# Optimization experiments

Measured on AMD Instinct MI355X. Metric: run time of the kernel, lower is better.

## Reference

```python
import jax, jax.numpy as jnp
import numpy as np

DIM = 512
NUM_HEADS = 8
HEAD_DIM = DIM // NUM_HEADS
SCALE = HEAD_DIM ** -0.5
B, N = 8, 1024


def setup_inputs() -> dict:
    key = jax.random.key(0)
    k1, k2, k3, k4, k5 = jax.random.split(key, 5)
    x = jax.random.normal(k1, (B, N, DIM), dtype=jnp.float32)
    rpe_bias = jax.random.normal(k2, (1, NUM_HEADS, N, N), dtype=jnp.float32)
    # torch Linear weights: [out_features, in_features], y = x @ W.T
    qkv_w = jax.random.normal(k3, (3 * DIM, DIM), dtype=jnp.float32) * (DIM ** -0.5)
    proj_w = jax.random.normal(k4, (DIM, DIM), dtype=jnp.float32) * (DIM ** -0.5)
    proj_b = jax.random.normal(k5, (DIM,), dtype=jnp.float32) * 0.01
    return {"x": x, "rpe_bias": rpe_bias, "qkv_w": qkv_w, "proj_w": proj_w, "proj_b": proj_b}


def reference(x, rpe_bias, qkv_w, proj_w, proj_b):
    b, n, c = x.shape
    h, d = NUM_HEADS, HEAD_DIM
    # qkv projection (no bias): [B,N,3C] -> [3,B,H,N,D]
    qkv = (x @ qkv_w.T).reshape(b, n, 3, h, d).transpose(2, 0, 3, 1, 4)
    q, k, v = qkv[0], qkv[1], qkv[2]
    attn = jnp.einsum('bhnd,bhmd->bhnm', q, k) * SCALE + rpe_bias
    attn = jax.nn.softmax(attn, axis=-1)  # dropout p=0 -> identity
    out = jnp.einsum('bhnm,bhmd->bhnd', attn, v)
    out = out.transpose(0, 2, 1, 3).reshape(b, n, c)
    return out @ proj_w.T + proj_b
```

## Files before the change

kernel.cpp:

```cpp
#include <hip/hip_runtime.h>
#include <hip/hip_bf16.h>

#define B_    8
#define N_    1024
#define DIM_  512
#define H_    8
#define DH_   64
#define SCALE_ 0.125f

typedef unsigned short u16;
typedef __attribute__((ext_vector_type(8))) short bf16x8;
typedef __attribute__((ext_vector_type(4))) float f32x4;

__device__ __forceinline__ u16 f2bf(float f) {
  union { float f; unsigned u; } v; v.f = f;
  return (u16)((v.u + 0x7fffu + ((v.u >> 16) & 1u)) >> 16);
}
__device__ __forceinline__ unsigned pack2(float a, float b) {
  return (unsigned)f2bf(a) | ((unsigned)f2bf(b) << 16);
}
__device__ __forceinline__ void cp16(const void* g, void* l) {
  __builtin_amdgcn_global_load_lds(
      (const __attribute__((address_space(1))) unsigned*)g,
      (__attribute__((address_space(3))) unsigned*)l, 16, 0, 0);
}

__global__ __launch_bounds__(256) void convert_kernel(
    const float* __restrict__ X, const float* __restrict__ Wq,
    const float* __restrict__ Wp, u16* __restrict__ Xb,
    u16* __restrict__ Wqb, u16* __restrict__ Wpb) {
  const int NX4 = (B_ * N_ * DIM_) / 4;
  const int NQ4 = (3 * DIM_ * DIM_) / 4;
  const int NP4 = (DIM_ * DIM_) / 4;
  const int total = NX4 + NQ4 + NP4;
  const int stride = gridDim.x * 256;
  for (int i = blockIdx.x * 256 + threadIdx.x; i < total; i += stride) {
    const float* s; u16* d; int off;
    if (i < NX4)            { s = X;  d = Xb;  off = i; }
    else if (i < NX4 + NQ4) { s = Wq; d = Wqb; off = i - NX4; }
    else                    { s = Wp; d = Wpb; off = i - NX4 - NQ4; }
    float4 f = *(const float4*)(s + (size_t)off * 4);
    uint2 u; u.x = pack2(f.x, f.y); u.y = pack2(f.z, f.w);
    *(uint2*)(d + (size_t)off * 4) = u;
  }
}

__global__ __launch_bounds__(256) void qkv_gemm(
    const u16* __restrict__ Ab, const u16* __restrict__ Bb,
    u16* __restrict__ Q, u16* __restrict__ K, u16* __restrict__ Vt) {
  __shared__ __align__(16) u16 sA[128 * 64];
  __shared__ __align__(16) u16 sB[128 * 64];
  const int t = threadIdx.x;
  const int wv = t >> 6, lane = t & 63, quad = (lane >> 4) & 3, l15 = lane & 15;
  const int wr = wv >> 1, wc = wv & 1;
  const int m0 = blockIdx.y * 128;
  const int n0 = blockIdx.x * 128;

  const int srow = lane >> 3;
  const int schunk = (lane & 7) ^ srow;
  const size_t ga = (size_t)(m0 + srow) * DIM_ + schunk * 8;
  const size_t gb = (size_t)(n0 + srow) * DIM_ + schunk * 8;

  f32x4 zero = {0.f, 0.f, 0.f, 0.f};
  f32x4 acc[4][4];
#pragma unroll
  for (int i = 0; i < 4; i++)
#pragma unroll
    for (int j = 0; j < 4; j++) acc[i][j] = zero;

  for (int k0 = 0; k0 < DIM_; k0 += 64) {
    __syncthreads();
#pragma unroll
    for (int i = 0; i < 4; i++) {
      const int rb = 32 * wv + 8 * i;
      cp16(Ab + ga + (size_t)rb * DIM_ + k0, &sA[rb * 64]);
      cp16(Bb + gb + (size_t)rb * DIM_ + k0, &sB[rb * 64]);
    }
    __syncthreads();
#pragma unroll
    for (int ks = 0; ks < 2; ks++) {
      bf16x8 af[4], bfv[4];
#pragma unroll
      for (int i = 0; i < 4; i++)
        af[i] = *(const bf16x8*)&sA[(wr * 64 + 16 * i + l15) * 64 +
                                    (((ks << 2) | quad) ^ (l15 & 7)) * 8];
#pragma unroll
      for (int j = 0; j < 4; j++)
        bfv[j] = *(const bf16x8*)&sB[(wc * 64 + 16 * j + l15) * 64 +
                                     (((ks << 2) | quad) ^ (l15 & 7)) * 8];
#pragma unroll
      for (int i = 0; i < 4; i++)
#pragma unroll
        for (int j = 0; j < 4; j++)
          acc[i][j] = __builtin_amdgcn_mfma_f32_16x16x32_bf16(af[i], bfv[j], acc[i][j], 0, 0, 0);
    }
  }

  const int tsel = n0 >> 9;
#pragma unroll
  for (int j = 0; j < 4; j++) {
    const int jg = n0 + wc * 64 + 16 * j + l15;
    const int h = (jg >> 6) & 7, d = jg & 63;
#pragma unroll
    for (int i = 0; i < 4; i++) {
      const int mbase = m0 + wr * 64 + 16 * i + quad * 4;
      const int b = mbase >> 10, nb = mbase & 1023;
      const size_t bh = (size_t)(b * H_ + h);
      if (tsel == 2) {
        ushort4 v4;
        v4.x = f2bf(acc[i][j][0]); v4.y = f2bf(acc[i][j][1]);
        v4.z = f2bf(acc[i][j][2]); v4.w = f2bf(acc[i][j][3]);
        *(ushort4*)&Vt[(bh * DH_ + d) * N_ + nb] = v4;
      } else {
        u16* dst = (tsel == 0 ? Q : K);
#pragma unroll
        for (int rr = 0; rr < 4; rr++)
          dst[(bh * N_ + nb + rr) * DH_ + d] = f2bf(acc[i][j][rr]);
      }
    }
  }
}

__global__ __launch_bounds__(256) void attn_kernel(
    const u16* __restrict__ Q, const u16* __restrict__ K,
    const u16* __restrict__ Vt, const float* __restrict__ bias,
    u16* __restrict__ AO) {
  __shared__ __align__(16) u16 sK[64 * 72];
  __shared__ __align__(16) u16 sV[64 * 72];
  __shared__ __align__(16) u16 sP[64 * 72];
  const int t = threadIdx.x;
  const int wv = t >> 6, lane = t & 63, quad = (lane >> 4) & 3, l15 = lane & 15;

  const int bid = blockIdx.x;
  const int h = bid & 7;
  const int s = bid >> 3;
  const int nx = s >> 3;
  const int b = s & 7;
  const int n0 = nx << 7;
  const int bh = b * H_ + h;
  const int r = t >> 2, c = (t & 3) << 4;

  const int qgA = n0 + 16 * wv + l15;
  const int qgB = qgA + 64;
  bf16x8 qfA0, qfA1, qfB0, qfB1;
  {
    const u16* qa = Q + (((size_t)bh << 10) + qgA) * DH_ + (quad << 3);
    const u16* qb = Q + (((size_t)bh << 10) + qgB) * DH_ + (quad << 3);
    qfA0 = *(const bf16x8*)qa; qfA1 = *(const bf16x8*)(qa + 32);
    qfB0 = *(const bf16x8*)qb; qfB1 = *(const bf16x8*)(qb + 32);
  }

  const float* bpA = bias + (((size_t)h << 10) + qgA) * N_ + (quad << 2);
  const float* bpB = bias + (((size_t)h << 10) + qgB) * N_ + (quad << 2);
  const u16* kbase = K + (((size_t)bh << 10) + r) * DH_ + c;
  const u16* vbase = Vt + (((size_t)bh << 6) + r) * N_ + c;

  f32x4 zero = {0.f, 0.f, 0.f, 0.f};
  f32x4 OA[4], OB[4];
#pragma unroll
  for (int i = 0; i < 4; i++) { OA[i] = zero; OB[i] = zero; }
  float lsumA = 0.f, lsumB = 0.f;

  uint4 k0r = *(const uint4*)kbase, k1r = *(const uint4*)(kbase + 8);
  uint4 v0r = *(const uint4*)vbase, v1r = *(const uint4*)(vbase + 8);

  for (int kt = 0; kt < 16; kt++) {
    const int m0k = kt << 6;
    __syncthreads();
    *(uint4*)&sK[r * 72 + c] = k0r;  *(uint4*)&sK[r * 72 + c + 8] = k1r;
    *(uint4*)&sV[r * 72 + c] = v0r;  *(uint4*)&sV[r * 72 + c + 8] = v1r;
    if (kt < 15) {
      const u16* kn = kbase + (size_t)(kt + 1) * 64 * DH_;
      const u16* vn = vbase + (kt + 1) * 64;
      k0r = *(const uint4*)kn; k1r = *(const uint4*)(kn + 8);
      v0r = *(const uint4*)vn; v1r = *(const uint4*)(vn + 8);
    }
    float4 bA[4], bB[4];
#pragma unroll
    for (int cb = 0; cb < 4; cb++) {
      bA[cb] = *(const float4*)(bpA + m0k + 16 * cb);
      bB[cb] = *(const float4*)(bpB + m0k + 16 * cb);
    }
    __syncthreads();

    bf16x8 kf[8];
#pragma unroll
    for (int ks = 0; ks < 2; ks++)
#pragma unroll
      for (int cb = 0; cb < 4; cb++)
        kf[ks * 4 + cb] =
            *(const bf16x8*)&sK[(16 * cb + l15) * 72 + ks * 32 + (quad << 3)];

    f32x4 SA[4], SB[4];
#pragma unroll
    for (int i = 0; i < 4; i++) { SA[i] = zero; SB[i] = zero; }
#pragma unroll
    for (int ks = 0; ks < 2; ks++) {
      const bf16x8 qa = ks ? qfA1 : qfA0;
      const bf16x8 qb = ks ? qfB1 : qfB0;
#pragma unroll
      for (int cb = 0; cb < 4; cb++) {
        SA[cb] = __builtin_amdgcn_mfma_f32_16x16x32_bf16(kf[ks * 4 + cb], qa, SA[cb], 0, 0, 0);
        SB[cb] = __builtin_amdgcn_mfma_f32_16x16x32_bf16(kf[ks * 4 + cb], qb, SB[cb], 0, 0, 0);
      }
    }

#pragma unroll
    for (int cb = 0; cb < 4; cb++) {
      float p0 = __expf(fmaf(SA[cb][0], SCALE_, bA[cb].x));
      float p1 = __expf(fmaf(SA[cb][1], SCALE_, bA[cb].y));
      float p2 = __expf(fmaf(SA[cb][2], SCALE_, bA[cb].z));
      float p3 = __expf(fmaf(SA[cb][3], SCALE_, bA[cb].w));
      lsumA += (p0 + p1) + (p2 + p3);
      uint2 pk; pk.x = pack2(p0, p1); pk.y = pack2(p2, p3);
      *(uint2*)&sP[(16 * wv + l15) * 72 + 16 * cb + (quad << 2)] = pk;
    }
    bf16x8 vf[8];
#pragma unroll
    for (int ks = 0; ks < 2; ks++)
#pragma unroll
      for (int cb = 0; cb < 4; cb++)
        vf[ks * 4 + cb] =
            *(const bf16x8*)&sV[(16 * cb + l15) * 72 + ks * 32 + (quad << 3)];
    asm volatile("s_waitcnt lgkmcnt(0)" ::: "memory");

#pragma unroll
    for (int ks = 0; ks < 2; ks++) {
      bf16x8 pf = *(const bf16x8*)&sP[(16 * wv + l15) * 72 + ks * 32 + (quad << 3)];
#pragma unroll
      for (int cb = 0; cb < 4; cb++)
        OA[cb] = __builtin_amdgcn_mfma_f32_16x16x32_bf16(vf[ks * 4 + cb], pf, OA[cb], 0, 0, 0);
    }

#pragma unroll
    for (int cb = 0; cb < 4; cb++) {
      float p0 = __expf(fmaf(SB[cb][0], SCALE_, bB[cb].x));
      float p1 = __expf(fmaf(SB[cb][1], SCALE_, bB[cb].y));
      float p2 = __expf(fmaf(SB[cb][2], SCALE_, bB[cb].z));
      float p3 = __expf(fmaf(SB[cb][3], SCALE_, bB[cb].w));
      lsumB += (p0 + p1) + (p2 + p3);
      uint2 pk; pk.x = pack2(p0, p1); pk.y = pack2(p2, p3);
      *(uint2*)&sP[(16 * wv + l15) * 72 + 16 * cb + (quad << 2)] = pk;
    }
    asm volatile("s_waitcnt lgkmcnt(0)" ::: "memory");
#pragma unroll
    for (int ks = 0; ks < 2; ks++) {
      bf16x8 pf = *(const bf16x8*)&sP[(16 * wv + l15) * 72 + ks * 32 + (quad << 3)];
#pragma unroll
      for (int cb = 0; cb < 4; cb++)
        OB[cb] = __builtin_amdgcn_mfma_f32_16x16x32_bf16(vf[ks * 4 + cb], pf, OB[cb], 0, 0, 0);
    }
  }

  lsumA += __shfl_xor(lsumA, 16); lsumA += __shfl_xor(lsumA, 32);
  lsumB += __shfl_xor(lsumB, 16); lsumB += __shfl_xor(lsumB, 32);
  const float invA = 1.f / lsumA, invB = 1.f / lsumB;
#pragma unroll
  for (int cb = 0; cb < 4; cb++) {
    ushort4 o4;
    o4.x = f2bf(OA[cb][0] * invA); o4.y = f2bf(OA[cb][1] * invA);
    o4.z = f2bf(OA[cb][2] * invA); o4.w = f2bf(OA[cb][3] * invA);
    *(ushort4*)&AO[(((size_t)b << 10) + qgA) * DIM_ + h * DH_ + 16 * cb + (quad << 2)] = o4;
    ushort4 p4;
    p4.x = f2bf(OB[cb][0] * invB); p4.y = f2bf(OB[cb][1] * invB);
    p4.z = f2bf(OB[cb][2] * invB); p4.w = f2bf(OB[cb][3] * invB);
    *(ushort4*)&AO[(((size_t)b << 10) + qgB) * DIM_ + h * DH_ + 16 * cb + (quad << 2)] = p4;
  }
}

__global__ __launch_bounds__(256) void proj_gemm(
    const u16* __restrict__ Ab, const u16* __restrict__ Bb,
    const float* __restrict__ Pb, float* __restrict__ Out) {
  __shared__ __align__(16) u16 sA[128 * 64];
  __shared__ __align__(16) u16 sB[128 * 64];
  const int t = threadIdx.x;
  const int wv = t >> 6, lane = t & 63, quad = (lane >> 4) & 3, l15 = lane & 15;
  const int wr = wv >> 1, wc = wv & 1;
  const int m0 = blockIdx.y * 128;
  const int n0 = blockIdx.x * 128;

  const int srow = lane >> 3;
  const int schunk = (lane & 7) ^ srow;
  const size_t ga = (size_t)(m0 + srow) * DIM_ + schunk * 8;
  const size_t gb = (size_t)(n0 + srow) * DIM_ + schunk * 8;

  f32x4 zero = {0.f, 0.f, 0.f, 0.f};
  f32x4 acc[4][4];
#pragma unroll
  for (int i = 0; i < 4; i++)
#pragma unroll
    for (int j = 0; j < 4; j++) acc[i][j] = zero;

  for (int k0 = 0; k0 < DIM_; k0 += 64) {
    __syncthreads();
#pragma unroll
    for (int i = 0; i < 4; i++) {
      const int rb = 32 * wv + 8 * i;
      cp16(Ab + ga + (size_t)rb * DIM_ + k0, &sA[rb * 64]);
      cp16(Bb + gb + (size_t)rb * DIM_ + k0, &sB[rb * 64]);
    }
    __syncthreads();
#pragma unroll
    for (int ks = 0; ks < 2; ks++) {
      bf16x8 af[4], bfv[4];
#pragma unroll
      for (int i = 0; i < 4; i++)
        af[i] = *(const bf16x8*)&sA[(wr * 64 + 16 * i + l15) * 64 +
                                    (((ks << 2) | quad) ^ (l15 & 7)) * 8];
#pragma unroll
      for (int j = 0; j < 4; j++)
        bfv[j] = *(const bf16x8*)&sB[(wc * 64 + 16 * j + l15) * 64 +
                                     (((ks << 2) | quad) ^ (l15 & 7)) * 8];
#pragma unroll
      for (int i = 0; i < 4; i++)
#pragma unroll
        for (int j = 0; j < 4; j++)
          acc[i][j] = __builtin_amdgcn_mfma_f32_16x16x32_bf16(af[i], bfv[j], acc[i][j], 0, 0, 0);
    }
  }

#pragma unroll
  for (int j = 0; j < 4; j++) {
    const int jg = n0 + wc * 64 + 16 * j + l15;
    const float pb = Pb[jg];
#pragma unroll
    for (int i = 0; i < 4; i++) {
      const int mbase = m0 + wr * 64 + 16 * i + quad * 4;
#pragma unroll
      for (int rr = 0; rr < 4; rr++)
        Out[(size_t)(mbase + rr) * DIM_ + jg] = acc[i][j][rr] + pb;
    }
  }
}

extern "C" void kernel_launch(void* const* d_in, const int* in_sizes, int n_in,
                              void* d_out, int out_size, void* d_ws, size_t ws_size,
                              hipStream_t stream) {
  const float* x      = (const float*)d_in[0];
  const float* rpe    = (const float*)d_in[1];
  const float* qkv_w  = (const float*)d_in[2];
  const float* proj_w = (const float*)d_in[3];
  const float* proj_b = (const float*)d_in[4];
  float* out = (float*)d_out;

  const size_t perbuf = (size_t)B_ * N_ * DIM_;
  u16* Xb  = (u16*)d_ws;
  u16* Q   = Xb + perbuf;
  u16* K   = Q + perbuf;
  u16* Vt  = K + perbuf;
  u16* Wqb = Vt + perbuf;
  u16* Wpb = Wqb + (size_t)3 * DIM_ * DIM_;
  u16* AO  = Xb;

  convert_kernel<<<2560, 256, 0, stream>>>(x, qkv_w, proj_w, Xb, Wqb, Wpb);
  qkv_gemm<<<dim3(12, 64), 256, 0, stream>>>(Xb, Wqb, Q, K, Vt);
  attn_kernel<<<512, 256, 0, stream>>>(Q, K, Vt, rpe, AO);
  proj_gemm<<<dim3(4, 64), 256, 0, stream>>>(AO, Wpb, proj_b, out);
}
```

Measured before the change: 174.6 us.

## Double-buffer K/V LDS tiles with XOR swizzle and MFMA priority hints

Splits the K/V shared-memory tiles into two buffers so the next tile is written while the current one is consumed. This drops one of the two barriers per iteration. The padded 72-element row stride is replaced by a 64-element stride with an XOR swizzle to avoid LDS bank conflicts, and s_setprio is raised around the MFMA blocks. LDS use grows from three tiles to five, which may reduce occupancy.

```diff
diff --git a/kernel.cpp b/kernel.cpp
--- a/kernel.cpp
+++ b/kernel.cpp
@@ -125,9 +125,9 @@
     const u16* __restrict__ Q, const u16* __restrict__ K,
     const u16* __restrict__ Vt, const float* __restrict__ bias,
     u16* __restrict__ AO) {
-  __shared__ __align__(16) u16 sK[64 * 72];
-  __shared__ __align__(16) u16 sV[64 * 72];
-  __shared__ __align__(16) u16 sP[64 * 72];
+  __shared__ __align__(16) u16 sK[2][64 * 64];
+  __shared__ __align__(16) u16 sV[2][64 * 64];
+  __shared__ __align__(16) u16 sP[64 * 64];
   const int t = threadIdx.x;
   const int wv = t >> 6, lane = t & 63, quad = (lane >> 4) & 3, l15 = lane & 15;
 
@@ -155,6 +155,12 @@
   const u16* kbase = K + (((size_t)bh << 10) + r) * DH_ + c;
   const u16* vbase = Vt + (((size_t)bh << 6) + r) * N_ + c;
 
+  const int so0 = r * 128 + ((((t & 3) << 5)) ^ ((r & 7) << 4));
+  const int so1 = r * 128 + ((((t & 3) << 5) + 16) ^ ((r & 7) << 4));
+  const int rx = (l15 & 7) << 4;
+  const int frow = l15 * 128;
+  const int prow = (16 * wv + l15) * 128;
+
   f32x4 zero = {0.f, 0.f, 0.f, 0.f};
   f32x4 OA[4], OB[4];
 #pragma unroll
@@ -163,37 +169,49 @@
 
   uint4 k0r = *(const uint4*)kbase, k1r = *(const uint4*)(kbase + 8);
   uint4 v0r = *(const uint4*)vbase, v1r = *(const uint4*)(vbase + 8);
+  *(uint4*)((char*)sK[0] + so0) = k0r; *(uint4*)((char*)sK[0] + so1) = k1r;
+  *(uint4*)((char*)sV[0] + so0) = v0r; *(uint4*)((char*)sV[0] + so1) = v1r;
+  {
+    const u16* kn = kbase + (size_t)64 * DH_;
+    const u16* vn = vbase + 64;
+    k0r = *(const uint4*)kn; k1r = *(const uint4*)(kn + 8);
+    v0r = *(const uint4*)vn; v1r = *(const uint4*)(vn + 8);
+  }
+  __syncthreads();
 
   for (int kt = 0; kt < 16; kt++) {
-    const int m0k = kt << 6;
-    __syncthreads();
-    *(uint4*)&sK[r * 72 + c] = k0r;  *(uint4*)&sK[r * 72 + c + 8] = k1r;
-    *(uint4*)&sV[r * 72 + c] = v0r;  *(uint4*)&sV[r * 72 + c + 8] = v1r;
+    const u16* cK = sK[kt & 1];
+    const u16* cV = sV[kt & 1];
     if (kt < 15) {
-      const u16* kn = kbase + (size_t)(kt + 1) * 64 * DH_;
-      const u16* vn = vbase + (kt + 1) * 64;
-      k0r = *(const uint4*)kn; k1r = *(const uint4*)(kn + 8);
-      v0r = *(const uint4*)vn; v1r = *(const uint4*)(vn + 8);
+      u16* wK = sK[(kt & 1) ^ 1]; u16* wV = sV[(kt & 1) ^ 1];
+      *(uint4*)((char*)wK + so0) = k0r; *(uint4*)((char*)wK + so1) = k1r;
+      *(uint4*)((char*)wV + so0) = v0r; *(uint4*)((char*)wV + so1) = v1r;
+      if (kt < 14) {
+        const u16* kn = kbase + (size_t)(kt + 2) * 64 * DH_;
+        const u16* vn = vbase + (kt + 2) * 64;
+        k0r = *(const uint4*)kn; k1r = *(const uint4*)(kn + 8);
+        v0r = *(const uint4*)vn; v1r = *(const uint4*)(vn + 8);
+      }
     }
     float4 bA[4], bB[4];
 #pragma unroll
     for (int cb = 0; cb < 4; cb++) {
-      bA[cb] = *(const float4*)(bpA + m0k + 16 * cb);
-      bB[cb] = *(const float4*)(bpB + m0k + 16 * cb);
-    }
-    __syncthreads();
+      bA[cb] = *(const float4*)(bpA + (kt << 6) + 16 * cb);
+      bB[cb] = *(const float4*)(bpB + (kt << 6) + 16 * cb);
+    }
 
     bf16x8 kf[8];
 #pragma unroll
     for (int ks = 0; ks < 2; ks++)
 #pragma unroll
       for (int cb = 0; cb < 4; cb++)
-        kf[ks * 4 + cb] =
-            *(const bf16x8*)&sK[(16 * cb + l15) * 72 + ks * 32 + (quad << 3)];
+        kf[ks * 4 + cb] = *(const bf16x8*)((const char*)cK + cb * 2048 + frow +
+                                           (((ks << 6) | (quad << 4)) ^ rx));
 
     f32x4 SA[4], SB[4];
 #pragma unroll
     for (int i = 0; i < 4; i++) { SA[i] = zero; SB[i] = zero; }
+    __builtin_amdgcn_s_setprio(1);
 #pragma unroll
     for (int ks = 0; ks < 2; ks++) {
       const bf16x8 qa = ks ? qfA1 : qfA0;
@@ -204,6 +222,7 @@
         SB[cb] = __builtin_amdgcn_mfma_f32_16x16x32_bf16(kf[ks * 4 + cb], qb, SB[cb], 0, 0, 0);
       }
     }
+    __builtin_amdgcn_s_setprio(0);
 
 #pragma unroll
     for (int cb = 0; cb < 4; cb++) {
@@ -213,24 +232,27 @@
       float p3 = __expf(fmaf(SA[cb][3], SCALE_, bA[cb].w));
       lsumA += (p0 + p1) + (p2 + p3);
       uint2 pk; pk.x = pack2(p0, p1); pk.y = pack2(p2, p3);
-      *(uint2*)&sP[(16 * wv + l15) * 72 + 16 * cb + (quad << 2)] = pk;
+      *(uint2*)((char*)sP + prow + (((cb << 5) | (quad << 3)) ^ rx)) = pk;
     }
     bf16x8 vf[8];
 #pragma unroll
     for (int ks = 0; ks < 2; ks++)
 #pragma unroll
       for (int cb = 0; cb < 4; cb++)
-        vf[ks * 4 + cb] =
-            *(const bf16x8*)&sV[(16 * cb + l15) * 72 + ks * 32 + (quad << 3)];
+        vf[ks * 4 + cb] = *(const bf16x8*)((const char*)cV + cb * 2048 + frow +
+                                           (((ks << 6) | (quad << 4)) ^ rx));
     asm volatile("s_waitcnt lgkmcnt(0)" ::: "memory");
 
-#pragma unroll
-    for (int ks = 0; ks < 2; ks++) {
-      bf16x8 pf = *(const bf16x8*)&sP[(16 * wv + l15) * 72 + ks * 32 + (quad << 3)];
+    __builtin_amdgcn_s_setprio(1);
+#pragma unroll
+    for (int ks = 0; ks < 2; ks++) {
+      bf16x8 pf = *(const bf16x8*)((const char*)sP + prow +
+                                   (((ks << 6) | (quad << 4)) ^ rx));
 #pragma unroll
       for (int cb = 0; cb < 4; cb++)
         OA[cb] = __builtin_amdgcn_mfma_f32_16x16x32_bf16(vf[ks * 4 + cb], pf, OA[cb], 0, 0, 0);
     }
+    __builtin_amdgcn_s_setprio(0);
 
 #pragma unroll
     for (int cb = 0; cb < 4; cb++) {
@@ -240,16 +262,20 @@
       float p3 = __expf(fmaf(SB[cb][3], SCALE_, bB[cb].w));
       lsumB += (p0 + p1) + (p2 + p3);
       uint2 pk; pk.x = pack2(p0, p1); pk.y = pack2(p2, p3);
-      *(uint2*)&sP[(16 * wv + l15) * 72 + 16 * cb + (quad << 2)] = pk;
+      *(uint2*)((char*)sP + prow + (((cb << 5) | (quad << 3)) ^ rx)) = pk;
     }
     asm volatile("s_waitcnt lgkmcnt(0)" ::: "memory");
-#pragma unroll
-    for (int ks = 0; ks < 2; ks++) {
-      bf16x8 pf = *(const bf16x8*)&sP[(16 * wv + l15) * 72 + ks * 32 + (quad << 3)];
+    __builtin_amdgcn_s_setprio(1);
+#pragma unroll
+    for (int ks = 0; ks < 2; ks++) {
+      bf16x8 pf = *(const bf16x8*)((const char*)sP + prow +
+                                   (((ks << 6) | (quad << 4)) ^ rx));
 #pragma unroll
       for (int cb = 0; cb < 4; cb++)
         OB[cb] = __builtin_amdgcn_mfma_f32_16x16x32_bf16(vf[ks * 4 + cb], pf, OB[cb], 0, 0, 0);
     }
+    __builtin_amdgcn_s_setprio(0);
+    __syncthreads();
   }
 
   lsumA += __shfl_xor(lsumA, 16); lsumA += __shfl_xor(lsumA, 32);
```

Result: no change. 177.3 us (+1.6%).
